# Kernel optimization log

Measured on AMD Instinct MI355X. Metric: run time of the kernel, lower is better.

Reference implementation:

```python
import jax, jax.numpy as jnp
import numpy as np

H = 16      # num_heads
D = 64      # hidden_size per head
IN = 1024   # input_size = H*D
B, S = 4, 2048

def setup_inputs() -> dict:
    key = jax.random.key(0)
    ks = jax.random.split(key, 5)
    scale = 1.0 / np.sqrt(IN)
    return {
        "x": jax.random.normal(ks[0], (B, S, IN), dtype=jnp.float32),
        "Wq": jax.random.normal(ks[1], (IN, H * D), dtype=jnp.float32) * scale,
        "bq": jnp.zeros((H * D,), dtype=jnp.float32),
        "Wk": jax.random.normal(ks[2], (IN, H * D), dtype=jnp.float32) * scale,
        "bk": jnp.zeros((H * D,), dtype=jnp.float32),
        "Wv": jax.random.normal(ks[3], (IN, H * D), dtype=jnp.float32) * scale,
        "bv": jnp.zeros((H * D,), dtype=jnp.float32),
        "Wo": jax.random.normal(ks[4], (H * D, IN), dtype=jnp.float32) * scale,
        "bo": jnp.zeros((IN,), dtype=jnp.float32),
    }

def reference(x, Wq, bq, Wk, bk, Wv, bv, Wo, bo):
    b, s, _ = x.shape
    # projections -> [b, h, s, d]
    def split_heads(t):
        return t.reshape(b, s, H, D).transpose(0, 2, 1, 3)
    q = split_heads(x @ Wq + bq)
    k = split_heads(x @ Wk + bk)
    v = split_heads(x @ Wv + bv)
    scores = jnp.einsum('bhqd,bhkd->bhqk', q, k) / jnp.sqrt(jnp.float32(D))
    probs = jax.nn.softmax(scores, axis=-1)            # [b,h,s,s]
    attn = jnp.einsum('bhqk,bhkd->bhqd', probs, v)     # [b,h,s,d]
    attn = attn.transpose(0, 2, 1, 3).reshape(b, s, H * D)
    out = attn @ Wo + bo
    return out, jnp.mean(probs, axis=1)
```

## Files before the change

### kernel.cpp

```cpp
#include <hip/hip_runtime.h>

typedef __attribute__((ext_vector_type(8))) short s8v;
typedef __attribute__((ext_vector_type(4))) short s4v;
typedef __attribute__((ext_vector_type(4))) float f4v;

#define DEV __device__ __forceinline__

DEV short b16(float f) {
  unsigned u = __builtin_bit_cast(unsigned, f);
  u = (u + 0x7fffu + ((u >> 16) & 1u)) >> 16;
  return (short)u;
}

DEV unsigned pk2(float a, float b) {
#if __has_builtin(__builtin_amdgcn_cvt_pk_bf16_f32)
  auto p = __builtin_amdgcn_cvt_pk_bf16_f32(a, b);
  return __builtin_bit_cast(unsigned, p);
#else
  return (unsigned)(unsigned short)b16(a) | ((unsigned)(unsigned short)b16(b) << 16);
#endif
}

DEV float fexp2(float x) {
#if __has_builtin(__builtin_amdgcn_exp2f)
  return __builtin_amdgcn_exp2f(x);
#else
  return exp2f(x);
#endif
}

DEV void gl_lds16(const short* g, short* l) {
  __builtin_amdgcn_global_load_lds((const __attribute__((address_space(1))) void*)g,
                                   (__attribute__((address_space(3))) void*)l, 16, 0, 0);
}

#define WAIT_VM(N) asm volatile("s_waitcnt vmcnt(" #N ")" ::: "memory")
#define WAIT_LGKM0() asm volatile("s_waitcnt lgkmcnt(0)" ::: "memory")
#define BAR() __builtin_amdgcn_s_barrier()

__global__ __launch_bounds__(256) void cast_f32_bf16(const float* __restrict__ in,
                                                     short* __restrict__ out, int n4) {
  int i = blockIdx.x * 256 + threadIdx.x;
  if (i >= n4) return;
  float4 v = ((const float4*)in)[i];
  s4v o; o.x = b16(v.x); o.y = b16(v.y); o.z = b16(v.z); o.w = b16(v.w);
  ((s4v*)out)[i] = o;
}

__global__ __launch_bounds__(256) void wtrans4(const float* __restrict__ W0, const float* __restrict__ W1,
                                               const float* __restrict__ W2, const float* __restrict__ W3,
                                               short* __restrict__ Wt) {
  const int mat = blockIdx.y;
  const float* W = mat == 0 ? W0 : (mat == 1 ? W1 : (mat == 2 ? W2 : W3));
  short* out = Wt + (long)mat * 1048576;
  int id = blockIdx.x * 256 + threadIdx.x;
  int k8 = id >> 10;
  int n  = id & 1023;
  s8v o;
#pragma unroll
  for (int j = 0; j < 8; ++j) o[j] = b16(W[(k8 * 8 + j) * 1024 + n]);
  *(s8v*)&out[n * 1024 + k8 * 8] = o;
}

__global__ __launch_bounds__(256) void gemm_qkv(const short* __restrict__ A,
                                                const short* __restrict__ Wt,
                                                const float* __restrict__ bq,
                                                const float* __restrict__ bk,
                                                const float* __restrict__ bv,
                                                short* __restrict__ Cb,
                                                short* __restrict__ Vt, float qscale) {
  __shared__ short AB[16384];
  short* As = AB;
  short* Bs = AB + 8192;
  int n = blockIdx.x + 24 * blockIdx.y;
  int id = (n & 7) * 192 + (n >> 3);
  const int nx = id % 24, my = id / 24;
  const int mat = nx >> 3;
  const short* Bt = Wt + (long)mat * 1048576;
  const float* bias = mat == 0 ? bq : (mat == 1 ? bk : bv);
  short* Cout = Cb + (long)mat * 8388608;
  const float scale = mat == 0 ? qscale : 1.0f;
  const int m0 = my * 128, n0 = (nx & 7) * 128;
  const int tid = threadIdx.x;
  const int w = tid >> 6, lane = tid & 63, quad = lane >> 4, l15 = lane & 15;
  const int wm = w >> 1, wn = w & 1;
  const int lr = lane >> 3, lc = (lane & 7) * 8;
  f4v acc[4][4] = {};
  for (int k0 = 0; k0 < 1024; k0 += 64) {
#pragma unroll
    for (int i = 0; i < 4; ++i) {
      int c = i * 4 + w;
      int r = c * 8 + lr;
      gl_lds16(&A[(m0 + r) * 1024 + k0 + lc], &As[c * 512]);
      gl_lds16(&Bt[(n0 + r) * 1024 + k0 + lc], &Bs[c * 512]);
    }
    __syncthreads();
#pragma unroll
    for (int kk = 0; kk < 2; ++kk) {
      s8v af[4], bf[4];
#pragma unroll
      for (int mt = 0; mt < 4; ++mt) af[mt] = *(const s8v*)&As[(wm * 64 + mt * 16 + l15) * 64 + kk * 32 + quad * 8];
#pragma unroll
      for (int nt = 0; nt < 4; ++nt) bf[nt] = *(const s8v*)&Bs[(wn * 64 + nt * 16 + l15) * 64 + kk * 32 + quad * 8];
#pragma unroll
      for (int mt = 0; mt < 4; ++mt)
#pragma unroll
        for (int nt = 0; nt < 4; ++nt)
          acc[mt][nt] = __builtin_amdgcn_mfma_f32_16x16x32_bf16(af[mt], bf[nt], acc[mt][nt], 0, 0, 0);
    }
    __syncthreads();
  }
  if (mat == 2) {
    short* T = AB;
#pragma unroll
    for (int nt = 0; nt < 4; ++nt) {
      const int c = wn * 64 + nt * 16 + l15;
      const float bcol = bias[n0 + c];
#pragma unroll
      for (int mt = 0; mt < 4; ++mt) {
        const int sr = wm * 64 + mt * 16 + quad * 4;
#pragma unroll
        for (int r = 0; r < 4; ++r) {
          int s = sr + r;
          T[c * 128 + ((((s >> 3) ^ (c & 15))) << 3) + (s & 7)] = b16(acc[mt][nt][r] + bcol);
        }
      }
    }
    __syncthreads();
    const int b = m0 >> 11, s0 = m0 & 2047, h0 = n0 >> 6;
#pragma unroll
    for (int i = 0; i < 8; ++i) {
      int unit = tid + i * 256;
      int c = unit >> 4, s8 = unit & 15;
      s8v v = *(const s8v*)&T[c * 128 + ((s8 ^ (c & 15)) << 3)];
      *(s8v*)&Vt[(((long)(b * 16 + h0 + (c >> 6)) * 64) + (c & 63)) * 2048 + s0 + s8 * 8] = v;
    }
  } else {
#pragma unroll
    for (int nt = 0; nt < 4; ++nt) {
      const int col = n0 + wn * 64 + nt * 16 + l15;
      const float bcol = bias[col];
#pragma unroll
      for (int mt = 0; mt < 4; ++mt)
#pragma unroll
        for (int r = 0; r < 4; ++r) {
          const int row = m0 + wm * 64 + mt * 16 + quad * 4 + r;
          Cout[row * 1024 + col] = b16((acc[mt][nt][r] + bcol) * scale);
        }
    }
  }
}

__global__ __launch_bounds__(256) void gemm128(const short* __restrict__ A,
                                               const short* __restrict__ Bt,
                                               const float* __restrict__ bias,
                                               float* __restrict__ Cout) {
  __shared__ short As[128 * 64];
  __shared__ short Bs[128 * 64];
  int n = blockIdx.x + 8 * blockIdx.y;
  int id = (n & 7) * 64 + (n >> 3);
  const int m0 = (id >> 3) * 128, n0 = (id & 7) * 128;
  const int tid = threadIdx.x;
  const int w = tid >> 6, lane = tid & 63, quad = lane >> 4, l15 = lane & 15;
  const int wm = w >> 1, wn = w & 1;
  const int lr = lane >> 3, lc = (lane & 7) * 8;
  f4v acc[4][4] = {};
  for (int k0 = 0; k0 < 1024; k0 += 64) {
#pragma unroll
    for (int i = 0; i < 4; ++i) {
      int c = i * 4 + w;
      int r = c * 8 + lr;
      gl_lds16(&A[(m0 + r) * 1024 + k0 + lc], &As[c * 512]);
      gl_lds16(&Bt[(n0 + r) * 1024 + k0 + lc], &Bs[c * 512]);
    }
    __syncthreads();
#pragma unroll
    for (int kk = 0; kk < 2; ++kk) {
      s8v af[4], bf[4];
#pragma unroll
      for (int mt = 0; mt < 4; ++mt) af[mt] = *(const s8v*)&As[(wm * 64 + mt * 16 + l15) * 64 + kk * 32 + quad * 8];
#pragma unroll
      for (int nt = 0; nt < 4; ++nt) bf[nt] = *(const s8v*)&Bs[(wn * 64 + nt * 16 + l15) * 64 + kk * 32 + quad * 8];
#pragma unroll
      for (int mt = 0; mt < 4; ++mt)
#pragma unroll
        for (int nt = 0; nt < 4; ++nt)
          acc[mt][nt] = __builtin_amdgcn_mfma_f32_16x16x32_bf16(af[mt], bf[nt], acc[mt][nt], 0, 0, 0);
    }
    __syncthreads();
  }
#pragma unroll
  for (int nt = 0; nt < 4; ++nt) {
    const int col = n0 + wn * 64 + nt * 16 + l15;
    const float bcol = bias[col];
#pragma unroll
    for (int mt = 0; mt < 4; ++mt)
#pragma unroll
      for (int r = 0; r < 4; ++r) {
        const int row = m0 + wm * 64 + mt * 16 + quad * 4 + r;
        Cout[row * 1024 + col] = acc[mt][nt][r] + bcol;
      }
  }
}

__global__ __launch_bounds__(256, 3) void attn_ctx(const short* __restrict__ Q, const short* __restrict__ K,
                                                   const short* __restrict__ Vt,
                                                   float* __restrict__ rbuf, short* __restrict__ ctx) {
  __shared__ __align__(16) char smem[49152];
  short* Ks = (short*)smem;
  short* Vs = (short*)(smem + 16384);
  short* Ps = (short*)(smem + 32768);
  short* Qs = Ps;
  int nlin = blockIdx.x + 32 * (blockIdx.y + 16 * blockIdx.z);
  int bid = (nlin & 7) * 256 + (nlin >> 3);
  const int q64 = bid & 31, h = (bid >> 5) & 15, b = bid >> 9;
  const int tid = threadIdx.x, w = tid >> 6, lane = tid & 63, quad = lane >> 4, l15 = lane & 15;
  const int bh = b * 16 + h, q0 = q64 * 64;

#pragma unroll
  for (int i = 0; i < 2; ++i) {
    int c = tid + i * 256;
    int r = c >> 3, cc = c & 7;
    *(s8v*)&Qs[r * 64 + (((cc ^ (r & 7))) << 3)] =
        *(const s8v*)&Q[((b * 2048 + q0 + r) * 16 + h) * 64 + cc * 8];
  }
  __syncthreads();
  s8v qf[4][2];
#pragma unroll
  for (int nt = 0; nt < 4; ++nt) {
    int r = nt * 16 + l15;
    qf[nt][0] = *(const s8v*)&Qs[r * 64 + ((quad ^ (r & 7)) << 3)];
    qf[nt][1] = *(const s8v*)&Qs[r * 64 + (((4 + quad) ^ (r & 7)) << 3)];
  }
  const short* kbase = &K[((long)(b * 2048) * 16 + h) * 64];
  const short* vbase = &Vt[(long)(bh * 64) * 2048];
  const int krow = w * 8 + (lane >> 3);
  const short* ksrc = kbase + krow * 1024 + (((lane & 7) ^ (lane >> 3)) << 3);
  const int vrow = w * 4 + (lane >> 4);
  const short* vsrc = vbase + vrow * 2048 + (((lane & 15) ^ vrow) << 3);
  f4v o[4] = {};
  f4v lf = {};
  s8v ones;
#pragma unroll
  for (int j = 0; j < 8; ++j) ones[j] = (short)0x3F80;

#pragma unroll
  for (int i = 0; i < 4; ++i) gl_lds16(ksrc + i * 32768, &Ks[(i * 4 + w) * 512]);
#pragma unroll
  for (int i = 0; i < 4; ++i) gl_lds16(vsrc + i * 32768, &Vs[(i * 4 + w) * 512]);
  WAIT_LGKM0();

  for (int kt = 0; kt < 16; ++kt) {
    WAIT_VM(4);
    BAR();
#pragma unroll
    for (int mt = 0; mt < 2; ++mt) {
      int kr = w * 32 + mt * 16 + l15;
      s8v a0 = *(const s8v*)&Ks[kr * 64 + ((quad ^ (kr & 7)) << 3)];
      s8v a1 = *(const s8v*)&Ks[kr * 64 + (((4 + quad) ^ (kr & 7)) << 3)];
#pragma unroll
      for (int nt = 0; nt < 4; ++nt) {
        f4v st = {};
        st = __builtin_amdgcn_mfma_f32_16x16x32_bf16(a0, qf[nt][0], st, 0, 0, 0);
        st = __builtin_amdgcn_mfma_f32_16x16x32_bf16(a1, qf[nt][1], st, 0, 0, 0);
        float e0 = fexp2(st[0]), e1 = fexp2(st[1]);
        float e2 = fexp2(st[2]), e3 = fexp2(st[3]);
        uint2 pp; pp.x = pk2(e0, e1); pp.y = pk2(e2, e3);
        int q = nt * 16 + l15;
        int chunk = (w * 4 + mt * 2 + (quad >> 1)) ^ l15;
        *(uint2*)&Ps[q * 128 + (chunk << 3) + (quad & 1) * 4] = pp;
      }
    }
    WAIT_LGKM0();
    BAR();
    if (kt < 15) {
#pragma unroll
      for (int i = 0; i < 4; ++i) gl_lds16(ksrc + (kt + 1) * 131072 + i * 32768, &Ks[(i * 4 + w) * 512]);
      WAIT_VM(4);
    } else {
      WAIT_VM(0);
    }
    BAR();
#pragma unroll
    for (int kk = 0; kk < 4; ++kk) {
      int qr = w * 16 + l15;
      s8v a = *(const s8v*)&Ps[qr * 128 + (((kk * 4 + quad) ^ (qr & 15)) << 3)];
#pragma unroll
      for (int dt = 0; dt < 4; ++dt) {
        int d = dt * 16 + l15;
        s8v vb = *(const s8v*)&Vs[d * 128 + (((kk * 4 + quad) ^ (d & 15)) << 3)];
        o[dt] = __builtin_amdgcn_mfma_f32_16x16x32_bf16(a, vb, o[dt], 0, 0, 0);
      }
      lf = __builtin_amdgcn_mfma_f32_16x16x32_bf16(a, ones, lf, 0, 0, 0);
    }
    WAIT_LGKM0();
    BAR();
    if (kt < 15) {
#pragma unroll
      for (int i = 0; i < 4; ++i) gl_lds16(vsrc + (kt + 1) * 128 + i * 32768, &Vs[(i * 4 + w) * 512]);
    }
  }

  float rv[4];
#pragma unroll
  for (int r = 0; r < 4; ++r) rv[r] = 1.0f / lf[r];
  if (l15 == 0) {
    f4v t; t[0] = rv[0]; t[1] = rv[1]; t[2] = rv[2]; t[3] = rv[3];
    *(f4v*)&rbuf[bh * 2048 + q0 + w * 16 + quad * 4] = t;
  }
#pragma unroll
  for (int dt = 0; dt < 4; ++dt)
#pragma unroll
    for (int r = 0; r < 4; ++r) {
      int sq = q0 + w * 16 + quad * 4 + r;
      ctx[((b * 2048 + sq) * 16 + h) * 64 + dt * 16 + l15] = b16(o[dt][r] * rv[r]);
    }
}

__global__ __launch_bounds__(256) void mean_probs(const short* __restrict__ Q, const short* __restrict__ K,
                                                  const float* __restrict__ rbuf, float* __restrict__ outm) {
  __shared__ __align__(16) short Qs[2][8192];
  __shared__ __align__(16) short Ks[2][8192];
  __shared__ __align__(16) float r_all[2048];
  int nlin = blockIdx.x + 16 * (blockIdx.y + 16 * blockIdx.z);
  int bid = (nlin & 7) * 128 + (nlin >> 3);
  const int k128 = bid & 15, q128 = (bid >> 4) & 15, b = bid >> 8;
  const int tid = threadIdx.x, w = tid >> 6, lane = tid & 63, quad = lane >> 4, l15 = lane & 15;
  f4v mn[2][8] = {};
  const int mrow = w * 8 + (lane >> 3);
  const int mck8 = ((lane & 7) ^ (lane >> 3)) << 3;
  const short* qsrc = Q + ((long)(b * 2048 + q128 * 128 + mrow) * 16) * 64 + mck8;
  const short* ksrc = K + ((long)(b * 2048 + k128 * 128 + mrow) * 16) * 64 + mck8;
  const float* rb = rbuf + (long)(b * 16) * 2048 + q128 * 128;
#pragma unroll
  for (int i = 0; i < 2; ++i) {
    int hh = i * 8 + w * 2 + (lane >> 5);
    gl_lds16((const short*)(rb + hh * 2048 + (lane & 31) * 4), (short*)r_all + (i * 4 + w) * 512);
  }
#pragma unroll
  for (int i = 0; i < 4; ++i) gl_lds16(qsrc + i * 32768, &Qs[0][(i * 4 + w) * 512]);
#pragma unroll
  for (int i = 0; i < 4; ++i) gl_lds16(ksrc + i * 32768, &Ks[0][(i * 4 + w) * 512]);

  for (int h = 0; h < 16; ++h) {
    const int cur = h & 1;
    WAIT_VM(0);
    BAR();
    if (h < 15) {
#pragma unroll
      for (int i = 0; i < 4; ++i) gl_lds16(qsrc + (h + 1) * 64 + i * 32768, &Qs[cur ^ 1][(i * 4 + w) * 512]);
#pragma unroll
      for (int i = 0; i < 4; ++i) gl_lds16(ksrc + (h + 1) * 64 + i * 32768, &Ks[cur ^ 1][(i * 4 + w) * 512]);
    }
    s8v aq[2][2];
#pragma unroll
    for (int qt = 0; qt < 2; ++qt) {
      int r = w * 32 + qt * 16 + l15;
      aq[qt][0] = *(const s8v*)&Qs[cur][r * 64 + ((quad ^ (r & 7)) << 3)];
      aq[qt][1] = *(const s8v*)&Qs[cur][r * 64 + (((4 + quad) ^ (r & 7)) << 3)];
    }
    float rr[2][4];
#pragma unroll
    for (int qt = 0; qt < 2; ++qt)
#pragma unroll
      for (int r = 0; r < 4; ++r) rr[qt][r] = r_all[h * 128 + w * 32 + qt * 16 + quad * 4 + r];
#pragma unroll
    for (int ktile = 0; ktile < 8; ++ktile) {
      int kr = ktile * 16 + l15;
      s8v b0 = *(const s8v*)&Ks[cur][kr * 64 + ((quad ^ (kr & 7)) << 3)];
      s8v b1 = *(const s8v*)&Ks[cur][kr * 64 + (((4 + quad) ^ (kr & 7)) << 3)];
#pragma unroll
      for (int qt = 0; qt < 2; ++qt) {
        f4v sc = {};
        sc = __builtin_amdgcn_mfma_f32_16x16x32_bf16(aq[qt][0], b0, sc, 0, 0, 0);
        sc = __builtin_amdgcn_mfma_f32_16x16x32_bf16(aq[qt][1], b1, sc, 0, 0, 0);
#pragma unroll
        for (int r = 0; r < 4; ++r)
          mn[qt][ktile][r] += fexp2(sc[r]) * rr[qt][r];
      }
    }
  }
#pragma unroll
  for (int qt = 0; qt < 2; ++qt)
#pragma unroll
    for (int ktile = 0; ktile < 8; ++ktile)
#pragma unroll
      for (int r = 0; r < 4; ++r) {
        long qrow = q128 * 128 + w * 32 + qt * 16 + quad * 4 + r;
        outm[((long)b * 2048 + qrow) * 2048 + k128 * 128 + ktile * 16 + l15] = mn[qt][ktile][r] * 0.0625f;
      }
}

extern "C" void kernel_launch(void* const* d_in, const int* in_sizes, int n_in,
                              void* d_out, int out_size, void* d_ws, size_t ws_size,
                              hipStream_t stream) {
  (void)in_sizes; (void)n_in; (void)out_size; (void)ws_size;
  const float* x  = (const float*)d_in[0];
  const float* Wq = (const float*)d_in[1];
  const float* bq = (const float*)d_in[2];
  const float* Wk = (const float*)d_in[3];
  const float* bk = (const float*)d_in[4];
  const float* Wv = (const float*)d_in[5];
  const float* bv = (const float*)d_in[6];
  const float* Wo = (const float*)d_in[7];
  const float* bo = (const float*)d_in[8];
  float* out  = (float*)d_out;
  float* outm = out + 8388608;

  char* ws = (char*)d_ws;
  short* xb  = (short*)(ws);
  short* Wqt = (short*)(ws + 16777216);
  short* Wot = (short*)(ws + 23068672);
  short* Qb  = (short*)(ws + 25165824);
  short* Kb  = (short*)(ws + 41943040);
  short* Vt  = (short*)(ws + 75497472);
  float* rbuf = (float*)(ws + 58720256);
  short* ctx = xb;

  const float C2 = 0.18033688011112042f;

  cast_f32_bf16<<<8192, 256, 0, stream>>>(x, xb, 2097152);
  wtrans4<<<dim3(512, 4), 256, 0, stream>>>(Wq, Wk, Wv, Wo, Wqt);
  gemm_qkv<<<dim3(24, 64), 256, 0, stream>>>(xb, Wqt, bq, bk, bv, Qb, Vt, C2);
  attn_ctx<<<dim3(32, 16, 4), 256, 0, stream>>>(Qb, Kb, Vt, rbuf, ctx);
  mean_probs<<<dim3(16, 16, 4), 256, 0, stream>>>(Qb, Kb, rbuf, outm);
  gemm128<<<dim3(8, 64), 256, 0, stream>>>(ctx, Wot, bo, out);
}
```

Measured before the change: 414.3 us.

## Split attention PV by key slice per wave and reduce partial outputs in LDS

Reworks the attention-context kernel so each wave computes a PV product over its own key slice for all 64 queries, not all keys for 16 queries. This lets the wave that produced a P tile consume it, so the barrier between the score/exp phase and the PV phase becomes a compiler sched_barrier. Partial O and row-sum accumulators are reduced across waves with LDS atomics at the end. K is now loaded as contiguous per-wave row blocks, and the initial K/V prefetch is issued before the Q load. The cost is 4x more accumulator registers, which puts pressure on the 3-blocks-per-CU occupancy target, plus an LDS atomic reduction epilogue.

```diff
diff --git a/kernel.cpp b/kernel.cpp
--- a/kernel.cpp
+++ b/kernel.cpp
@@ -37,6 +37,7 @@
 #define WAIT_VM(N) asm volatile("s_waitcnt vmcnt(" #N ")" ::: "memory")
 #define WAIT_LGKM0() asm volatile("s_waitcnt lgkmcnt(0)" ::: "memory")
 #define BAR() __builtin_amdgcn_s_barrier()
+#define SBAR() __builtin_amdgcn_sched_barrier(0)
 
 __global__ __launch_bounds__(256) void cast_f32_bf16(const float* __restrict__ in,
                                                      short* __restrict__ out, int n4) {
@@ -211,12 +212,26 @@
   short* Vs = (short*)(smem + 16384);
   short* Ps = (short*)(smem + 32768);
   short* Qs = Ps;
+  float* OS  = (float*)smem;
+  float* LfS = (float*)(smem + 16384);
   int nlin = blockIdx.x + 32 * (blockIdx.y + 16 * blockIdx.z);
   int bid = (nlin & 7) * 256 + (nlin >> 3);
   const int q64 = bid & 31, h = (bid >> 5) & 15, b = bid >> 9;
   const int tid = threadIdx.x, w = tid >> 6, lane = tid & 63, quad = lane >> 4, l15 = lane & 15;
   const int bh = b * 16 + h, q0 = q64 * 64;
 
+  const short* kbase = &K[((long)(b * 2048) * 16 + h) * 64];
+  const short* vbase = &Vt[(long)(bh * 64) * 2048];
+  const int lr3 = lane >> 3;
+  const short* ksrc = kbase + (w * 32 + lr3) * 1024 + (((lane & 7) ^ lr3) << 3);
+  const int vrow = w * 4 + (lane >> 4);
+  const short* vsrc = vbase + vrow * 2048 + (((lane & 15) ^ vrow) << 3);
+
+#pragma unroll
+  for (int i = 0; i < 4; ++i) gl_lds16(ksrc + i * 8192, Ks + w * 2048 + i * 512);
+#pragma unroll
+  for (int i = 0; i < 4; ++i) gl_lds16(vsrc + i * 32768, Vs + (i * 4 + w) * 512);
+
 #pragma unroll
   for (int i = 0; i < 2; ++i) {
     int c = tid + i * 256;
@@ -232,27 +247,16 @@
     qf[nt][0] = *(const s8v*)&Qs[r * 64 + ((quad ^ (r & 7)) << 3)];
     qf[nt][1] = *(const s8v*)&Qs[r * 64 + (((4 + quad) ^ (r & 7)) << 3)];
   }
-  const short* kbase = &K[((long)(b * 2048) * 16 + h) * 64];
-  const short* vbase = &Vt[(long)(bh * 64) * 2048];
-  const int krow = w * 8 + (lane >> 3);
-  const short* ksrc = kbase + krow * 1024 + (((lane & 7) ^ (lane >> 3)) << 3);
-  const int vrow = w * 4 + (lane >> 4);
-  const short* vsrc = vbase + vrow * 2048 + (((lane & 15) ^ vrow) << 3);
-  f4v o[4] = {};
-  f4v lf = {};
+  WAIT_LGKM0(); SBAR();
+
+  f4v o[4][4] = {};
+  f4v lf[4] = {};
   s8v ones;
 #pragma unroll
   for (int j = 0; j < 8; ++j) ones[j] = (short)0x3F80;
 
-#pragma unroll
-  for (int i = 0; i < 4; ++i) gl_lds16(ksrc + i * 32768, &Ks[(i * 4 + w) * 512]);
-#pragma unroll
-  for (int i = 0; i < 4; ++i) gl_lds16(vsrc + i * 32768, &Vs[(i * 4 + w) * 512]);
-  WAIT_LGKM0();
-
   for (int kt = 0; kt < 16; ++kt) {
-    WAIT_VM(4);
-    BAR();
+    WAIT_VM(4); SBAR();
 #pragma unroll
     for (int mt = 0; mt < 2; ++mt) {
       int kr = w * 32 + mt * 16 + l15;
@@ -271,49 +275,77 @@
         *(uint2*)&Ps[q * 128 + (chunk << 3) + (quad & 1) * 4] = pp;
       }
     }
-    WAIT_LGKM0();
-    BAR();
+    WAIT_LGKM0(); SBAR();
     if (kt < 15) {
 #pragma unroll
-      for (int i = 0; i < 4; ++i) gl_lds16(ksrc + (kt + 1) * 131072 + i * 32768, &Ks[(i * 4 + w) * 512]);
+      for (int i = 0; i < 4; ++i)
+        gl_lds16(ksrc + (kt + 1) * 131072 + i * 8192, Ks + w * 2048 + i * 512);
       WAIT_VM(4);
     } else {
       WAIT_VM(0);
     }
+    SBAR();
     BAR();
-#pragma unroll
-    for (int kk = 0; kk < 4; ++kk) {
-      int qr = w * 16 + l15;
-      s8v a = *(const s8v*)&Ps[qr * 128 + (((kk * 4 + quad) ^ (qr & 15)) << 3)];
-#pragma unroll
-      for (int dt = 0; dt < 4; ++dt) {
-        int d = dt * 16 + l15;
-        s8v vb = *(const s8v*)&Vs[d * 128 + (((kk * 4 + quad) ^ (d & 15)) << 3)];
-        o[dt] = __builtin_amdgcn_mfma_f32_16x16x32_bf16(a, vb, o[dt], 0, 0, 0);
-      }
-      lf = __builtin_amdgcn_mfma_f32_16x16x32_bf16(a, ones, lf, 0, 0, 0);
-    }
-    WAIT_LGKM0();
+    s8v vb[4];
+#pragma unroll
+    for (int dt = 0; dt < 4; ++dt) {
+      int d = dt * 16 + l15;
+      vb[dt] = *(const s8v*)&Vs[d * 128 + (((w * 4 + quad) ^ (d & 15)) << 3)];
+    }
+#pragma unroll
+    for (int nt = 0; nt < 4; ++nt) {
+      int q = nt * 16 + l15;
+      s8v pa = *(const s8v*)&Ps[q * 128 + (((w * 4 + quad) ^ l15) << 3)];
+#pragma unroll
+      for (int dt = 0; dt < 4; ++dt)
+        o[nt][dt] = __builtin_amdgcn_mfma_f32_16x16x32_bf16(pa, vb[dt], o[nt][dt], 0, 0, 0);
+      lf[nt] = __builtin_amdgcn_mfma_f32_16x16x32_bf16(pa, ones, lf[nt], 0, 0, 0);
+    }
+    WAIT_LGKM0(); SBAR();
     BAR();
     if (kt < 15) {
 #pragma unroll
-      for (int i = 0; i < 4; ++i) gl_lds16(vsrc + (kt + 1) * 128 + i * 32768, &Vs[(i * 4 + w) * 512]);
-    }
-  }
-
-  float rv[4];
-#pragma unroll
-  for (int r = 0; r < 4; ++r) rv[r] = 1.0f / lf[r];
-  if (l15 == 0) {
-    f4v t; t[0] = rv[0]; t[1] = rv[1]; t[2] = rv[2]; t[3] = rv[3];
-    *(f4v*)&rbuf[bh * 2048 + q0 + w * 16 + quad * 4] = t;
-  }
+      for (int i = 0; i < 4; ++i)
+        gl_lds16(vsrc + (kt + 1) * 128 + i * 32768, Vs + (i * 4 + w) * 512);
+    }
+  }
+
+#pragma unroll
+  for (int j = 0; j < 4; ++j) ((f4v*)OS)[tid * 4 + j] = f4v{};
+  if (tid < 64) LfS[tid] = 0.f;
+  WAIT_LGKM0();
+  BAR();
+#pragma unroll
+  for (int nt = 0; nt < 4; ++nt) {
+#pragma unroll
+    for (int dt = 0; dt < 4; ++dt)
+#pragma unroll
+      for (int r = 0; r < 4; ++r)
+        atomicAdd(&OS[(nt * 16 + quad * 4 + r) * 64 + dt * 16 + l15], o[nt][dt][r]);
+    if (l15 == 0)
+#pragma unroll
+      for (int r = 0; r < 4; ++r)
+        atomicAdd(&LfS[nt * 16 + quad * 4 + r], lf[nt][r]);
+  }
+  WAIT_LGKM0();
+  BAR();
+  if (tid < 64) {
+    float rv = 1.0f / LfS[tid];
+    LfS[tid] = rv;
+    rbuf[bh * 2048 + q0 + tid] = rv;
+  }
+  WAIT_LGKM0();
+  BAR();
+  float rv4[4];
+#pragma unroll
+  for (int r = 0; r < 4; ++r) rv4[r] = LfS[w * 16 + quad * 4 + r];
 #pragma unroll
   for (int dt = 0; dt < 4; ++dt)
 #pragma unroll
     for (int r = 0; r < 4; ++r) {
-      int sq = q0 + w * 16 + quad * 4 + r;
-      ctx[((b * 2048 + sq) * 16 + h) * 64 + dt * 16 + l15] = b16(o[dt][r] * rv[r]);
+      int qloc = w * 16 + quad * 4 + r;
+      float val = OS[qloc * 64 + dt * 16 + l15] * rv4[r];
+      ctx[((b * 2048 + q0 + qloc) * 16 + h) * 64 + dt * 16 + l15] = b16(val);
     }
 }
 
```

After: 578.5 us. 1.4x slower.

## Double-buffer LDS tiles in QKV and output projection GEMMs

Applied to the files above, without the earlier changes.

Both projection GEMMs now hold two LDS stages and issue the global-to-LDS loads for the next K tile before computing on the current one, with one barrier per iteration instead of two. The goal is to hide global load latency behind MFMA work. LDS use per block doubles to 64KB, which can cut occupancy. It also relies on WAIT_VM/WAIT_LGKM0/BAR macros being defined in the hidden part of the file.

```diff
diff --git a/kernel.cpp b/kernel.cpp
--- a/kernel.cpp
+++ b/kernel.cpp
@@ -69,9 +69,7 @@
                                                 const float* __restrict__ bv,
                                                 short* __restrict__ Cb,
                                                 short* __restrict__ Vt, float qscale) {
-  __shared__ short AB[16384];
-  short* As = AB;
-  short* Bs = AB + 8192;
+  __shared__ short AB[32768];
   int n = blockIdx.x + 24 * blockIdx.y;
   int id = (n & 7) * 192 + (n >> 3);
   const int nx = id % 24, my = id / 24;
@@ -86,15 +84,31 @@
   const int wm = w >> 1, wn = w & 1;
   const int lr = lane >> 3, lc = (lane & 7) * 8;
   f4v acc[4][4] = {};
-  for (int k0 = 0; k0 < 1024; k0 += 64) {
-#pragma unroll
-    for (int i = 0; i < 4; ++i) {
-      int c = i * 4 + w;
-      int r = c * 8 + lr;
-      gl_lds16(&A[(m0 + r) * 1024 + k0 + lc], &As[c * 512]);
-      gl_lds16(&Bt[(n0 + r) * 1024 + k0 + lc], &Bs[c * 512]);
-    }
-    __syncthreads();
+#pragma unroll
+  for (int i = 0; i < 4; ++i) {
+    int c = i * 4 + w;
+    int r = c * 8 + lr;
+    gl_lds16(&A[(m0 + r) * 1024 + lc], &AB[c * 512]);
+    gl_lds16(&Bt[(n0 + r) * 1024 + lc], &AB[8192 + c * 512]);
+  }
+  for (int t = 0; t < 16; ++t) {
+    const int cur = (t & 1) * 16384;
+    WAIT_VM(0);
+    WAIT_LGKM0();
+    BAR();
+    if (t < 15) {
+      const int nxt = ((t + 1) & 1) * 16384;
+      const int k0 = (t + 1) * 64;
+#pragma unroll
+      for (int i = 0; i < 4; ++i) {
+        int c = i * 4 + w;
+        int r = c * 8 + lr;
+        gl_lds16(&A[(m0 + r) * 1024 + k0 + lc], &AB[nxt + c * 512]);
+        gl_lds16(&Bt[(n0 + r) * 1024 + k0 + lc], &AB[nxt + 8192 + c * 512]);
+      }
+    }
+    const short* As = &AB[cur];
+    const short* Bs = &AB[cur + 8192];
 #pragma unroll
     for (int kk = 0; kk < 2; ++kk) {
       s8v af[4], bf[4];
@@ -108,9 +122,9 @@
         for (int nt = 0; nt < 4; ++nt)
           acc[mt][nt] = __builtin_amdgcn_mfma_f32_16x16x32_bf16(af[mt], bf[nt], acc[mt][nt], 0, 0, 0);
     }
+  }
+  if (mat == 2) {
     __syncthreads();
-  }
-  if (mat == 2) {
     short* T = AB;
 #pragma unroll
     for (int nt = 0; nt < 4; ++nt) {
@@ -155,8 +169,7 @@
                                                const short* __restrict__ Bt,
                                                const float* __restrict__ bias,
                                                float* __restrict__ Cout) {
-  __shared__ short As[128 * 64];
-  __shared__ short Bs[128 * 64];
+  __shared__ short AB[32768];
   int n = blockIdx.x + 8 * blockIdx.y;
   int id = (n & 7) * 64 + (n >> 3);
   const int m0 = (id >> 3) * 128, n0 = (id & 7) * 128;
@@ -165,15 +178,31 @@
   const int wm = w >> 1, wn = w & 1;
   const int lr = lane >> 3, lc = (lane & 7) * 8;
   f4v acc[4][4] = {};
-  for (int k0 = 0; k0 < 1024; k0 += 64) {
-#pragma unroll
-    for (int i = 0; i < 4; ++i) {
-      int c = i * 4 + w;
-      int r = c * 8 + lr;
-      gl_lds16(&A[(m0 + r) * 1024 + k0 + lc], &As[c * 512]);
-      gl_lds16(&Bt[(n0 + r) * 1024 + k0 + lc], &Bs[c * 512]);
-    }
-    __syncthreads();
+#pragma unroll
+  for (int i = 0; i < 4; ++i) {
+    int c = i * 4 + w;
+    int r = c * 8 + lr;
+    gl_lds16(&A[(m0 + r) * 1024 + lc], &AB[c * 512]);
+    gl_lds16(&Bt[(n0 + r) * 1024 + lc], &AB[8192 + c * 512]);
+  }
+  for (int t = 0; t < 16; ++t) {
+    const int cur = (t & 1) * 16384;
+    WAIT_VM(0);
+    WAIT_LGKM0();
+    BAR();
+    if (t < 15) {
+      const int nxt = ((t + 1) & 1) * 16384;
+      const int k0 = (t + 1) * 64;
+#pragma unroll
+      for (int i = 0; i < 4; ++i) {
+        int c = i * 4 + w;
+        int r = c * 8 + lr;
+        gl_lds16(&A[(m0 + r) * 1024 + k0 + lc], &AB[nxt + c * 512]);
+        gl_lds16(&Bt[(n0 + r) * 1024 + k0 + lc], &AB[nxt + 8192 + c * 512]);
+      }
+    }
+    const short* As = &AB[cur];
+    const short* Bs = &AB[cur + 8192];
 #pragma unroll
     for (int kk = 0; kk < 2; ++kk) {
       s8v af[4], bf[4];
@@ -187,7 +216,6 @@
         for (int nt = 0; nt < 4; ++nt)
           acc[mt][nt] = __builtin_amdgcn_mfma_f32_16x16x32_bf16(af[mt], bf[nt], acc[mt][nt], 0, 0, 0);
     }
-    __syncthreads();
   }
 #pragma unroll
   for (int nt = 0; nt < 4; ++nt) {
```

New measurement: 401.1 us. 3.2% less time.
